# Kernel optimization log

Hardware: AMD Instinct MI355X
Metric: run time of the kernel (lower is better)

The kernel has to match this reference:

```python
import jax, jax.numpy as jnp
import numpy as np

N_EL = 4            # allowed elements (H, C, N, O)
N_EXPERTS = N_EL * N_EL
F_ATOM = 176        # per-atom symmetry feature dim
F_PAIR = 32         # pair feature dim (2*F_ATOM + F_PAIR == 384 == nodes[0])


def _init_linear(key, fin, fout, n):
    # torch nn.Linear default init: U(-1/sqrt(fin), 1/sqrt(fin))
    bound = 1.0 / np.sqrt(fin)
    kw, kb = jax.random.split(key)
    W = jax.random.uniform(kw, (n, fin, fout), minval=-bound, maxval=bound, dtype=jnp.float32)
    b = jax.random.uniform(kb, (n, fout), minval=-bound, maxval=bound, dtype=jnp.float32)
    return W, b


def setup_inputs() -> dict:
    key = jax.random.key(0)
    ks = jax.random.split(key, 8)
    B, A, C = 128, 128, 256
    elements = jax.random.randint(ks[0], (B, A), 0, N_EL)
    connectivity = jax.random.randint(ks[1], (B, C, 2), 0, A)
    sym_features = jax.random.normal(ks[2], (B, A, F_ATOM), dtype=jnp.float32)
    pair_features = jax.random.normal(ks[3], (B, C, F_PAIR), dtype=jnp.float32)
    W1, b1 = _init_linear(ks[4], 384, 128, N_EXPERTS)
    W2, b2 = _init_linear(ks[5], 128, 96, N_EXPERTS)
    W3, b3 = _init_linear(ks[6], 96, 2, N_EXPERTS)
    return dict(elements=elements, connectivity=connectivity,
                sym_features=sym_features, pair_features=pair_features,
                W1=W1, b1=b1, W2=W2, b2=b2, W3=W3, b3=b3)


def _pair_moe(elements, connectivity, sym_features, pair_features, W1, b1, W2, b2, W3, b3):
    B, C, _ = connectivity.shape
    A = sym_features.shape[1]
    out_dim = W3.shape[-1]

    # mirror: mask padded pairs (connectivity[...,0] == -1) before offsetting
    mask = (connectivity[..., 0] != -1).reshape(-1)              # [B*C]
    conn_f = (connectivity + (jnp.arange(B) * A)[:, None, None]).reshape(-1, 2)
    idx0 = jnp.where(mask, conn_f[:, 0], 0)
    idx1 = jnp.where(mask, conn_f[:, 1], 0)

    feat_f = sym_features.reshape(-1, sym_features.shape[-1])    # [B*A, F]
    el_f = elements.reshape(-1)                                  # [B*A]

    m = mask[:, None].astype(sym_features.dtype)
    fa = feat_f[idx0] * m                                        # [B*C, F] (zeros where padded)
    fb = feat_f[idx1] * m
    e0 = jnp.where(mask, el_f[idx0], -1)
    e1 = jnp.where(mask, el_f[idx1], -1)
    nn_index = e0 * N_EL + e1                                    # -5 for padded pairs -> no expert

    x = jnp.concatenate([fa, fb, pair_features.reshape(-1, pair_features.shape[-1])], axis=1)

    y = jnp.zeros((x.shape[0], out_dim), dtype=x.dtype)
    for i in range(N_EXPERTS):  # fixed small expert set (structural loop)
        h = jax.nn.celu(x @ W1[i] + b1[i])
        h = jax.nn.celu(h @ W2[i] + b2[i])
        o = h @ W3[i] + b3[i]
        y = jnp.where((nn_index == i)[:, None], o, y)
    return y.reshape(B, C, out_dim)


def reference(elements, connectivity, sym_features, pair_features, W1, b1, W2, b2, W3, b3):
    # Original returns (elements, connectivity, y); only y is computed output.
    return _pair_moe(elements, connectivity, sym_features, pair_features, W1, b1, W2, b2, W3, b3)
```

## Files before the change

### kernel.cpp

```cpp
#include <hip/hip_runtime.h>
#include <math.h>

typedef __attribute__((ext_vector_type(8))) short short8;
typedef __attribute__((ext_vector_type(4))) float f32x4;

namespace {
constexpr int NEL   = 4;
constexpr int NEXP  = 16;
constexpr int Bb    = 128;
constexpr int Aa    = 128;
constexpr int Cc    = 256;
constexpr int FATOM = 176;
constexpr int FPAIR = 32;
constexpr int FIN   = 384;
constexpr int HH1   = 128;
constexpr int HH2   = 96;
constexpr int NP    = Bb * Cc;
constexpr int BUCKET_CAP = 4096;

constexpr int WS_COUNTS = 0;
constexpr int WS_BUCKET = 64;
constexpr int WS_SHORTS = 65600;

constexpr int W2_OFF = 12 * HH1 * 32;
constexpr int WPK_E  = W2_OFF + 4 * HH2 * 32;
constexpr int WPK_N  = NEXP * WPK_E;

constexpr int SYM_N  = Bb * Aa * FATOM;
constexpr int PAIR_N = Bb * Cc * FPAIR;

constexpr int CVT_BLOCKS = (SYM_N / 4 + PAIR_N / 4) / 256;
constexpr int W1_BLOCKS  = 768;
constexpr int W2_BLOCKS  = 192;
constexpr int IDX_BLOCKS = NP / 256;
constexpr int W1_BASE  = CVT_BLOCKS;
constexpr int W2_BASE  = W1_BASE + W1_BLOCKS;
constexpr int IDX_BASE = W2_BASE + W2_BLOCKS;
constexpr int PREP_GRID = IDX_BASE + IDX_BLOCKS;
}

__device__ inline short f2bf(float f) {
    unsigned u = __builtin_bit_cast(unsigned, f);
    unsigned r = (u + 0x7FFFu + ((u >> 16) & 1u)) >> 16;
    return (short)r;
}
__device__ inline float celu1(float v) {
    return v > 0.f ? v : (__expf(v) - 1.0f);
}

__global__ __launch_bounds__(256) void k_prep(
    const float* __restrict__ sym, const float* __restrict__ pairf,
    short* __restrict__ symb, short* __restrict__ pairfb,
    const float* __restrict__ W1, const float* __restrict__ W2,
    short* __restrict__ wpk,
    const int* __restrict__ conn, const int* __restrict__ elements,
    int* __restrict__ counts, int* __restrict__ bucket,
    float* __restrict__ out)
{
    __shared__ float T[32][33];
    __shared__ int sh_cnt[NEXP], sh_base[NEXP];

    int bid = blockIdx.x;
    int t = threadIdx.x;

    if (bid < CVT_BLOCKS) {
        int i = bid * 256 + t;
        constexpr int NS4 = SYM_N / 4;
        const float4* src; short* dst; int j;
        if (i < NS4) { src = (const float4*)sym;   dst = symb;   j = i; }
        else         { src = (const float4*)pairf; dst = pairfb; j = i - NS4; }
        float4 v = src[j];
        short4 o;
        o.x = f2bf(v.x); o.y = f2bf(v.y); o.z = f2bf(v.z); o.w = f2bf(v.w);
        *(short4*)(dst + 4 * (size_t)j) = o;
    } else if (bid < IDX_BASE) {
        const float* src; short* dst; int N, k0, n0;
        if (bid < W2_BASE) {
            int b1i = bid - W1_BASE;
            int e = b1i / 48, tl = b1i % 48;
            N = HH1; k0 = (tl % 12) * 32; n0 = (tl / 12) * 32;
            src = W1 + (size_t)e * FIN * HH1;
            dst = wpk + (size_t)e * WPK_E;
        } else {
            int b2i = bid - W2_BASE;
            int e = b2i / 12, tl = b2i % 12;
            N = HH2; k0 = (tl % 4) * 32; n0 = (tl / 4) * 32;
            src = W2 + (size_t)e * HH1 * HH2;
            dst = wpk + (size_t)e * WPK_E + W2_OFF;
        }
        int tx = t & 31, ty = t >> 5;
        int ks = k0 >> 5;
#pragma unroll
        for (int j = 0; j < 4; ++j) {
            int r = ty + 8 * j;
            T[r][tx] = src[(size_t)(k0 + r) * N + n0 + tx];
        }
        __syncthreads();
#pragma unroll
        for (int j = 0; j < 4; ++j) {
            int n = n0 + ty + 8 * j;
            dst[(size_t)(ks * N + n) * 32 + tx] = f2bf(T[tx][ty + 8 * j]);
        }
    } else {
        int p = (bid - IDX_BASE) * 256 + t;
        if (t < NEXP) sh_cnt[t] = 0;
        __syncthreads();
        int e = -1, r = 0;
        {
            int c0 = conn[2 * p], c1 = conn[2 * p + 1];
            if (c0 != -1) {
                int b = p / Cc;
                int i0 = b * Aa + c0; if (i0 < 0) i0 += Bb * Aa;
                int i1 = b * Aa + c1; if (i1 < 0) i1 += Bb * Aa;
                e = elements[i0] * NEL + elements[i1];
            }
            if (e < 0 || e >= NEXP) {
                out[2 * p] = 0.f; out[2 * p + 1] = 0.f;
                e = -1;
            } else {
                r = atomicAdd(&sh_cnt[e], 1);
            }
        }
        __syncthreads();
        if (t < NEXP) sh_base[t] = (sh_cnt[t] > 0) ? atomicAdd(&counts[t], sh_cnt[t]) : 0;
        __syncthreads();
        if (e >= 0) {
            int pos = sh_base[e] + r;
            if (pos < BUCKET_CAP) bucket[e * BUCKET_CAP + pos] = p;
        }
    }
}

#define PAIR_PTRS(P)                                                          \
    int2 c = ((const int2*)conn)[P];                                          \
    int bb = ((P) >> 8) << 7;                                                 \
    const short* fa = symb + (size_t)(bb + (c.x & 127)) * FATOM;              \
    const short* fb = symb + (size_t)(bb + (c.y & 127)) * FATOM;              \
    const short* pf = pairfb + (size_t)(P) * FPAIR;

#define GATHER()                                                              \
    a0  = *(const short8*)(fa + 8 * lg);                                      \
    a1  = *(const short8*)(fa + 32 + 8 * lg);                                 \
    a2  = *(const short8*)(fa + 64 + 8 * lg);                                 \
    a3  = *(const short8*)(fa + 96 + 8 * lg);                                 \
    a4  = *(const short8*)(fa + 128 + 8 * lg);                                \
    a5  = *(const short8*)((lg < 2 ? fa + 160 : fb - 16) + 8 * lg);           \
    a6  = *(const short8*)(fb + 16 + 8 * lg);                                 \
    a7  = *(const short8*)(fb + 48 + 8 * lg);                                 \
    a8  = *(const short8*)(fb + 80 + 8 * lg);                                 \
    a9  = *(const short8*)(fb + 112 + 8 * lg);                                \
    a10 = *(const short8*)(fb + 144 + 8 * lg);                                \
    a11 = *(const short8*)(pf + 8 * lg);

#define L1K(A, KS)                                                            \
    _Pragma("unroll")                                                         \
    for (int j = 0; j < 8; ++j) {                                             \
        short8 bw = *(const short8*)&Wlds[((KS) * HH1 + j * 16 + lr) * 32 + 8 * lg]; \
        acc[j] = __builtin_amdgcn_mfma_f32_16x16x32_bf16(A, bw, acc[j], 0, 0, 0); \
    }

__global__ __launch_bounds__(512, 2) void k_moe(
    const int* __restrict__ counts, const int* __restrict__ bucket,
    const int* __restrict__ conn,
    const short* __restrict__ symb, const short* __restrict__ pairfb,
    const short* __restrict__ wpk,
    const float* __restrict__ b1, const float* __restrict__ b2,
    const float* __restrict__ W3, const float* __restrict__ b3,
    float* __restrict__ out)
{
    __shared__ short Wlds[WPK_E];
    __shared__ short H1s[8][16 * HH1];

    int e     = blockIdx.x & 15;
    int shard = blockIdx.x >> 4;
    int cnt = counts[e];
    if (cnt > BUCKET_CAP) cnt = BUCKET_CAP;
    int nt = (cnt + 15) >> 4;

    int t = threadIdx.x;
    int w = t >> 6;
    int lane = t & 63;
    int lr = lane & 15, lg = (lane >> 4) & 3;

    const int* bucket_e = bucket + e * BUCKET_CAP;
    const short* wsrc = wpk + (size_t)e * WPK_E;

    int tile = shard * 8 + w;
    int ii = tile * 16 + lr;
    int idx0 = ii < cnt ? ii : (cnt > 0 ? cnt - 1 : 0);
    int p = bucket_e[idx0] & (NP - 1);
    short8 a0, a1, a2, a3, a4, a5, a6, a7, a8, a9, a10, a11;
    {
        PAIR_PTRS(p)
        GATHER()
    }
    __builtin_amdgcn_sched_barrier(0);

    short8 v[15];
#pragma unroll
    for (int r = 0; r < 15; ++r) v[r] = *(const short8*)(wsrc + r * 4096 + t * 8);
    float b1v[8];
#pragma unroll
    for (int j = 0; j < 8; ++j) b1v[j] = b1[e * HH1 + j * 16 + lr];
    float2 b3v = ((const float2*)b3)[e];
    __builtin_amdgcn_sched_barrier(0);

#pragma unroll
    for (int r = 0; r < 15; ++r) *(short8*)&Wlds[r * 4096 + t * 8] = v[r];
    __syncthreads();

    short* h1w = &H1s[w][0];

    for (;;) {
        f32x4 acc[8];
#pragma unroll
        for (int j = 0; j < 8; ++j) acc[j] = (f32x4){b1v[j], b1v[j], b1v[j], b1v[j]};
        L1K(a0, 0)  L1K(a1, 1)  L1K(a2, 2)  L1K(a3, 3)
        L1K(a4, 4)  L1K(a5, 5)  L1K(a6, 6)  L1K(a7, 7)
        L1K(a8, 8)  L1K(a9, 9)  L1K(a10, 10) L1K(a11, 11)

#pragma unroll
        for (int j = 0; j < 8; ++j)
#pragma unroll
            for (int r2 = 0; r2 < 4; ++r2) {
                int m = 4 * lg + r2;
                int n = 16 * j + lr;
                h1w[m * HH1 + (((n >> 3) ^ (m & 7)) << 3) + (n & 7)] = f2bf(celu1(acc[j][r2]));
            }
        asm volatile("s_waitcnt lgkmcnt(0)" ::: "memory");
        __builtin_amdgcn_sched_barrier(0);

        int mx = lr & 7;
        short8 bh0 = *(const short8*)&h1w[lr * HH1 + (((0 + lg) ^ mx) << 3)];
        short8 bh1 = *(const short8*)&h1w[lr * HH1 + (((4 + lg) ^ mx) << 3)];
        short8 bh2 = *(const short8*)&h1w[lr * HH1 + (((8 + lg) ^ mx) << 3)];
        short8 bh3 = *(const short8*)&h1w[lr * HH1 + (((12 + lg) ^ mx) << 3)];

        float s0 = 0.f, s1 = 0.f;
#pragma unroll
        for (int t6 = 0; t6 < 6; ++t6) {
            int n2b = 16 * t6 + 4 * lg;
            float4 bb4 = *(const float4*)&b2[e * HH2 + n2b];
            f32x4 a2c;
            a2c[0] = bb4.x; a2c[1] = bb4.y; a2c[2] = bb4.z; a2c[3] = bb4.w;
            {
                short8 aw = *(const short8*)&Wlds[W2_OFF + (0 * HH2 + 16 * t6 + lr) * 32 + 8 * lg];
                a2c = __builtin_amdgcn_mfma_f32_16x16x32_bf16(aw, bh0, a2c, 0, 0, 0);
            }
            {
                short8 aw = *(const short8*)&Wlds[W2_OFF + (1 * HH2 + 16 * t6 + lr) * 32 + 8 * lg];
                a2c = __builtin_amdgcn_mfma_f32_16x16x32_bf16(aw, bh1, a2c, 0, 0, 0);
            }
            {
                short8 aw = *(const short8*)&Wlds[W2_OFF + (2 * HH2 + 16 * t6 + lr) * 32 + 8 * lg];
                a2c = __builtin_amdgcn_mfma_f32_16x16x32_bf16(aw, bh2, a2c, 0, 0, 0);
            }
            {
                short8 aw = *(const short8*)&Wlds[W2_OFF + (3 * HH2 + 16 * t6 + lr) * 32 + 8 * lg];
                a2c = __builtin_amdgcn_mfma_f32_16x16x32_bf16(aw, bh3, a2c, 0, 0, 0);
            }
            float4 w3a = *(const float4*)&W3[(size_t)(e * HH2 + n2b) * 2];
            float4 w3b = *(const float4*)&W3[(size_t)(e * HH2 + n2b) * 2 + 4];
            float h0 = celu1(a2c[0]), h1c = celu1(a2c[1]), h2 = celu1(a2c[2]), h3 = celu1(a2c[3]);
            s0 = fmaf(h0, w3a.x, fmaf(h1c, w3a.z, fmaf(h2, w3b.x, fmaf(h3, w3b.z, s0))));
            s1 = fmaf(h0, w3a.y, fmaf(h1c, w3a.w, fmaf(h2, w3b.y, fmaf(h3, w3b.w, s1))));
        }
        s0 += __shfl_xor(s0, 16); s0 += __shfl_xor(s0, 32);
        s1 += __shfl_xor(s1, 16); s1 += __shfl_xor(s1, 32);
        if (((lane >> 4) & 3) == 0 && ii < cnt && tile < nt) {
            float2 o2; o2.x = s0 + b3v.x; o2.y = s1 + b3v.y;
            *(float2*)(out + 2 * (size_t)bucket_e[ii]) = o2;
        }

        tile += 128;
        if (tile >= nt) break;
        ii = tile * 16 + lr;
        int idx = ii < cnt ? ii : cnt - 1;
        p = bucket_e[idx] & (NP - 1);
        PAIR_PTRS(p)
        GATHER()
    }
}

extern "C" void kernel_launch(void* const* d_in, const int* in_sizes, int n_in,
                              void* d_out, int out_size, void* d_ws, size_t ws_size,
                              hipStream_t stream)
{
    const int*   elements = (const int*)d_in[0];
    const int*   conn     = (const int*)d_in[1];
    const float* sym      = (const float*)d_in[2];
    const float* pairf    = (const float*)d_in[3];
    const float* W1       = (const float*)d_in[4];
    const float* b1       = (const float*)d_in[5];
    const float* W2       = (const float*)d_in[6];
    const float* b2       = (const float*)d_in[7];
    const float* W3       = (const float*)d_in[8];
    const float* b3       = (const float*)d_in[9];
    float* out = (float*)d_out;

    int* wsi    = (int*)d_ws;
    int* counts = wsi + WS_COUNTS;
    int* bucket = wsi + WS_BUCKET;

    short* sbase  = (short*)(wsi + WS_SHORTS);
    short* wpk    = sbase;
    short* symb   = sbase + WPK_N;
    short* pairfb = sbase + WPK_N + SYM_N;

    hipMemsetAsync((void*)counts, 0, NEXP * sizeof(int), stream);

    k_prep<<<PREP_GRID, 256, 0, stream>>>(sym, pairf, symb, pairfb,
                                          W1, W2, wpk,
                                          conn, elements, counts, bucket, out);
    k_moe<<<256, 512, 0, stream>>>(counts, bucket, conn, symb, pairfb, wpk,
                                   b1, b2, W3, b3, out);
}
```

Before: 37.08 us.

## Process two 16-row tiles per wave and store gather indices in bucket

Each wave now handles 32 pairs as two M-tiles that share every W1 fragment read from LDS, halving LDS weight traffic per pair in layer 1. The persistent loop is removed, so each wave does one 32-pair tile and exits, and inactive waves return after the weight load. The prep kernel stores int4 records holding the pair id and both atom indices, so the MoE kernel no longer reads connectivity before the feature gather. The cost is higher register pressure from 24 A fragments and two accumulator sets, and a correctness risk if 16 shards times 8 waves times 32 rows cannot cover a full bucket (4096 fits exactly).

```diff
diff --git a/kernel.cpp b/kernel.cpp
--- a/kernel.cpp
+++ b/kernel.cpp
@@ -16,18 +16,19 @@
 constexpr int HH1   = 128;
 constexpr int HH2   = 96;
 constexpr int NP    = Bb * Cc;
+constexpr int NA    = Bb * Aa;
 constexpr int BUCKET_CAP = 4096;
 
 constexpr int WS_COUNTS = 0;
-constexpr int WS_BUCKET = 64;
-constexpr int WS_SHORTS = 65600;
+constexpr int WS_B2     = 64;
+constexpr int WS_SHORTS = 64 + NEXP * BUCKET_CAP * 4;
 
 constexpr int W2_OFF = 12 * HH1 * 32;
 constexpr int WPK_E  = W2_OFF + 4 * HH2 * 32;
 constexpr int WPK_N  = NEXP * WPK_E;
 
-constexpr int SYM_N  = Bb * Aa * FATOM;
-constexpr int PAIR_N = Bb * Cc * FPAIR;
+constexpr int SYM_N  = NA * FATOM;
+constexpr int PAIR_N = NP * FPAIR;
 
 constexpr int CVT_BLOCKS = (SYM_N / 4 + PAIR_N / 4) / 256;
 constexpr int W1_BLOCKS  = 768;
@@ -54,7 +55,7 @@
     const float* __restrict__ W1, const float* __restrict__ W2,
     short* __restrict__ wpk,
     const int* __restrict__ conn, const int* __restrict__ elements,
-    int* __restrict__ counts, int* __restrict__ bucket,
+    int* __restrict__ counts, int4* __restrict__ bucket2,
     float* __restrict__ out)
 {
     __shared__ float T[32][33];
@@ -105,13 +106,13 @@
         int p = (bid - IDX_BASE) * 256 + t;
         if (t < NEXP) sh_cnt[t] = 0;
         __syncthreads();
-        int e = -1, r = 0;
+        int e = -1, r = 0, i0 = 0, i1 = 0;
         {
             int c0 = conn[2 * p], c1 = conn[2 * p + 1];
             if (c0 != -1) {
                 int b = p / Cc;
-                int i0 = b * Aa + c0; if (i0 < 0) i0 += Bb * Aa;
-                int i1 = b * Aa + c1; if (i1 < 0) i1 += Bb * Aa;
+                i0 = b * Aa + c0; if (i0 < 0) i0 += NA;
+                i1 = b * Aa + c1; if (i1 < 0) i1 += NA;
                 e = elements[i0] * NEL + elements[i1];
             }
             if (e < 0 || e >= NEXP) {
@@ -126,42 +127,34 @@
         __syncthreads();
         if (e >= 0) {
             int pos = sh_base[e] + r;
-            if (pos < BUCKET_CAP) bucket[e * BUCKET_CAP + pos] = p;
+            if (pos < BUCKET_CAP) {
+                int4 rec; rec.x = p; rec.y = i0; rec.z = i1; rec.w = 0;
+                bucket2[e * BUCKET_CAP + pos] = rec;
+            }
         }
     }
 }
 
-#define PAIR_PTRS(P)                                                          \
-    int2 c = ((const int2*)conn)[P];                                          \
-    int bb = ((P) >> 8) << 7;                                                 \
-    const short* fa = symb + (size_t)(bb + (c.x & 127)) * FATOM;              \
-    const short* fb = symb + (size_t)(bb + (c.y & 127)) * FATOM;              \
-    const short* pf = pairfb + (size_t)(P) * FPAIR;
-
-#define GATHER()                                                              \
-    a0  = *(const short8*)(fa + 8 * lg);                                      \
-    a1  = *(const short8*)(fa + 32 + 8 * lg);                                 \
-    a2  = *(const short8*)(fa + 64 + 8 * lg);                                 \
-    a3  = *(const short8*)(fa + 96 + 8 * lg);                                 \
-    a4  = *(const short8*)(fa + 128 + 8 * lg);                                \
-    a5  = *(const short8*)((lg < 2 ? fa + 160 : fb - 16) + 8 * lg);           \
-    a6  = *(const short8*)(fb + 16 + 8 * lg);                                 \
-    a7  = *(const short8*)(fb + 48 + 8 * lg);                                 \
-    a8  = *(const short8*)(fb + 80 + 8 * lg);                                 \
-    a9  = *(const short8*)(fb + 112 + 8 * lg);                                \
-    a10 = *(const short8*)(fb + 144 + 8 * lg);                                \
-    a11 = *(const short8*)(pf + 8 * lg);
-
-#define L1K(A, KS)                                                            \
-    _Pragma("unroll")                                                         \
-    for (int j = 0; j < 8; ++j) {                                             \
-        short8 bw = *(const short8*)&Wlds[((KS) * HH1 + j * 16 + lr) * 32 + 8 * lg]; \
-        acc[j] = __builtin_amdgcn_mfma_f32_16x16x32_bf16(A, bw, acc[j], 0, 0, 0); \
-    }
+#define GATHER2(A, REC) do {                                                  \
+    const short* fa = symb + (size_t)((REC).y & (NA - 1)) * FATOM;            \
+    const short* fb = symb + (size_t)((REC).z & (NA - 1)) * FATOM;            \
+    const short* pf = pairfb + (size_t)((REC).x & (NP - 1)) * FPAIR;          \
+    A[0]  = *(const short8*)(fa + 8 * lg);                                    \
+    A[1]  = *(const short8*)(fa + 32 + 8 * lg);                               \
+    A[2]  = *(const short8*)(fa + 64 + 8 * lg);                               \
+    A[3]  = *(const short8*)(fa + 96 + 8 * lg);                               \
+    A[4]  = *(const short8*)(fa + 128 + 8 * lg);                              \
+    A[5]  = *(const short8*)((lg < 2 ? fa + 160 : fb - 16) + 8 * lg);         \
+    A[6]  = *(const short8*)(fb + 16 + 8 * lg);                               \
+    A[7]  = *(const short8*)(fb + 48 + 8 * lg);                               \
+    A[8]  = *(const short8*)(fb + 80 + 8 * lg);                               \
+    A[9]  = *(const short8*)(fb + 112 + 8 * lg);                              \
+    A[10] = *(const short8*)(fb + 144 + 8 * lg);                              \
+    A[11] = *(const short8*)(pf + 8 * lg);                                    \
+} while (0)
 
 __global__ __launch_bounds__(512, 2) void k_moe(
-    const int* __restrict__ counts, const int* __restrict__ bucket,
-    const int* __restrict__ conn,
+    const int* __restrict__ counts, const int4* __restrict__ bucket2,
     const short* __restrict__ symb, const short* __restrict__ pairfb,
     const short* __restrict__ wpk,
     const float* __restrict__ b1, const float* __restrict__ b2,
@@ -175,25 +168,27 @@
     int shard = blockIdx.x >> 4;
     int cnt = counts[e];
     if (cnt > BUCKET_CAP) cnt = BUCKET_CAP;
-    int nt = (cnt + 15) >> 4;
+    int nt = (cnt + 31) >> 5;
 
     int t = threadIdx.x;
     int w = t >> 6;
     int lane = t & 63;
     int lr = lane & 15, lg = (lane >> 4) & 3;
 
-    const int* bucket_e = bucket + e * BUCKET_CAP;
+    const int4* b2e = bucket2 + e * BUCKET_CAP;
     const short* wsrc = wpk + (size_t)e * WPK_E;
 
-    int tile = shard * 8 + w;
-    int ii = tile * 16 + lr;
-    int idx0 = ii < cnt ? ii : (cnt > 0 ? cnt - 1 : 0);
-    int p = bucket_e[idx0] & (NP - 1);
-    short8 a0, a1, a2, a3, a4, a5, a6, a7, a8, a9, a10, a11;
-    {
-        PAIR_PTRS(p)
-        GATHER()
-    }
+    int tile = w * 16 + shard;
+    bool active = tile < nt;
+
+    int ii0 = tile * 32 + lr;
+    int ii1 = ii0 + 16;
+    int cm1 = cnt > 0 ? cnt - 1 : 0;
+    int4 rec0 = b2e[active ? (ii0 < cnt ? ii0 : cm1) : 0];
+    int4 rec1 = b2e[active ? (ii1 < cnt ? ii1 : cm1) : 0];
+    short8 aA[12], aB[12];
+    GATHER2(aA, rec0);
+    GATHER2(aB, rec1);
     __builtin_amdgcn_sched_barrier(0);
 
     short8 v[15];
@@ -209,23 +204,35 @@
     for (int r = 0; r < 15; ++r) *(short8*)&Wlds[r * 4096 + t * 8] = v[r];
     __syncthreads();
 
+    if (!active) return;
+
     short* h1w = &H1s[w][0];
 
-    for (;;) {
-        f32x4 acc[8];
-#pragma unroll
-        for (int j = 0; j < 8; ++j) acc[j] = (f32x4){b1v[j], b1v[j], b1v[j], b1v[j]};
-        L1K(a0, 0)  L1K(a1, 1)  L1K(a2, 2)  L1K(a3, 3)
-        L1K(a4, 4)  L1K(a5, 5)  L1K(a6, 6)  L1K(a7, 7)
-        L1K(a8, 8)  L1K(a9, 9)  L1K(a10, 10) L1K(a11, 11)
-
+    f32x4 acc[2][8];
+#pragma unroll
+    for (int j = 0; j < 8; ++j) {
+        acc[0][j] = (f32x4){b1v[j], b1v[j], b1v[j], b1v[j]};
+        acc[1][j] = acc[0][j];
+    }
+#pragma unroll
+    for (int ks = 0; ks < 12; ++ks) {
+#pragma unroll
+        for (int j = 0; j < 8; ++j) {
+            short8 bw = *(const short8*)&Wlds[(ks * HH1 + j * 16 + lr) * 32 + 8 * lg];
+            acc[0][j] = __builtin_amdgcn_mfma_f32_16x16x32_bf16(aA[ks], bw, acc[0][j], 0, 0, 0);
+            acc[1][j] = __builtin_amdgcn_mfma_f32_16x16x32_bf16(aB[ks], bw, acc[1][j], 0, 0, 0);
+        }
+    }
+
+#pragma unroll
+    for (int mi = 0; mi < 2; ++mi) {
 #pragma unroll
         for (int j = 0; j < 8; ++j)
 #pragma unroll
             for (int r2 = 0; r2 < 4; ++r2) {
                 int m = 4 * lg + r2;
                 int n = 16 * j + lr;
-                h1w[m * HH1 + (((n >> 3) ^ (m & 7)) << 3) + (n & 7)] = f2bf(celu1(acc[j][r2]));
+                h1w[m * HH1 + (((n >> 3) ^ (m & 7)) << 3) + (n & 7)] = f2bf(celu1(acc[mi][j][r2]));
             }
         asm volatile("s_waitcnt lgkmcnt(0)" ::: "memory");
         __builtin_amdgcn_sched_barrier(0);
@@ -267,18 +274,12 @@
         }
         s0 += __shfl_xor(s0, 16); s0 += __shfl_xor(s0, 32);
         s1 += __shfl_xor(s1, 16); s1 += __shfl_xor(s1, 32);
-        if (((lane >> 4) & 3) == 0 && ii < cnt && tile < nt) {
+        int ii = mi == 0 ? ii0 : ii1;
+        int pp = (mi == 0 ? rec0.x : rec1.x) & (NP - 1);
+        if (((lane >> 4) & 3) == 0 && ii < cnt) {
             float2 o2; o2.x = s0 + b3v.x; o2.y = s1 + b3v.y;
-            *(float2*)(out + 2 * (size_t)bucket_e[ii]) = o2;
-        }
-
-        tile += 128;
-        if (tile >= nt) break;
-        ii = tile * 16 + lr;
-        int idx = ii < cnt ? ii : cnt - 1;
-        p = bucket_e[idx] & (NP - 1);
-        PAIR_PTRS(p)
-        GATHER()
+            *(float2*)(out + 2 * (size_t)pp) = o2;
+        }
     }
 }
 
@@ -298,9 +299,9 @@
     const float* b3       = (const float*)d_in[9];
     float* out = (float*)d_out;
 
-    int* wsi    = (int*)d_ws;
-    int* counts = wsi + WS_COUNTS;
-    int* bucket = wsi + WS_BUCKET;
+    int* wsi     = (int*)d_ws;
+    int* counts  = wsi + WS_COUNTS;
+    int4* bucket2 = (int4*)(wsi + WS_B2);
 
     short* sbase  = (short*)(wsi + WS_SHORTS);
     short* wpk    = sbase;
@@ -311,7 +312,7 @@
 
     k_prep<<<PREP_GRID, 256, 0, stream>>>(sym, pairf, symb, pairfb,
                                           W1, W2, wpk,
-                                          conn, elements, counts, bucket, out);
-    k_moe<<<256, 512, 0, stream>>>(counts, bucket, conn, symb, pairfb, wpk,
+                                          conn, elements, counts, bucket2, out);
+    k_moe<<<256, 512, 0, stream>>>(counts, bucket2, symb, pairfb, wpk,
                                    b1, b2, W3, b3, out);
 }
```

New measurement: 32.02 us. 1.16x faster.
